# Kernel tuning notes

Measured on AMD Instinct MI355X. Metric: run time of the kernel, lower is better.

Reference implementation:

```python
import jax, jax.numpy as jnp
import numpy as np

B, L, S, D, H = 32, 256, 64, 128, 4
DH = D // H
EPS = 1e-5


def _uniform(k, shape, scale):
    return jax.random.uniform(k, shape, jnp.float32, -scale, scale)


def setup_inputs() -> dict:
    key = jax.random.key(0)
    ks = jax.random.split(key, 12)
    sc = 1.0 / np.sqrt(D)
    return {
        "h_wq": jax.random.normal(ks[0], (B, L, D), jnp.float32),
        "h_all": jax.random.normal(ks[1], (B, L, S, D), jnp.float32),
        "station_id": jax.random.randint(ks[2], (B,), 0, S),
        "adj": jax.random.randint(ks[3], (S, S), 0, 2).astype(jnp.float32),
        "in_proj_w": _uniform(ks[4], (3 * D, D), sc),
        "in_proj_b": _uniform(ks[5], (3 * D,), sc),
        "out_w": _uniform(ks[6], (D, D), sc),
        "out_b": _uniform(ks[7], (D,), sc),
        "gate_w": _uniform(ks[8], (D, 2 * D), 1.0 / np.sqrt(2 * D)),
        "gate_b": _uniform(ks[9], (D,), 1.0 / np.sqrt(2 * D)),
        "ln_g": jnp.ones((D,), jnp.float32),
        "ln_b": jnp.zeros((D,), jnp.float32),
        "alpha": jnp.asarray(0.1, jnp.float32),
    }


def _allowed_mask(adj, station_id):
    # allowed[b, s] == True  <=> station s may attend as key for sample b
    sid = station_id.astype(jnp.int32)
    allowed = adj[sid] > 0.0                                  # [B, S]
    self_oh = jax.nn.one_hot(sid, adj.shape[0], dtype=bool)   # [B, S]
    allowed = allowed & ~self_oh                              # exclude self
    # fallback-to-all for rows with no neighbor (still excluding self)
    no_nb = ~jnp.any(allowed, axis=1, keepdims=True)
    allowed = jnp.where(no_nb, ~self_oh, allowed)
    # final safety: if STILL empty (S==1 edge case), allow self
    no_nb2 = ~jnp.any(allowed, axis=1, keepdims=True)
    allowed = allowed | (no_nb2 & self_oh)
    return allowed


def _forward(h_wq, h_all, station_id, adj, in_proj_w, in_proj_b,
             out_w, out_b, gate_w, gate_b, ln_g, ln_b, alpha):
    b, l, d = h_wq.shape
    s = h_all.shape[2]
    qw, kw, vw = jnp.split(in_proj_w, 3, axis=0)
    qb, kb, vb = jnp.split(in_proj_b, 3, axis=0)

    q = (h_wq @ qw.T + qb).reshape(b, l, H, DH)        # [B,L,H,DH]
    k = (h_all @ kw.T + kb).reshape(b, l, s, H, DH)    # [B,L,S,H,DH]
    v = (h_all @ vw.T + vb).reshape(b, l, s, H, DH)

    scores = jnp.einsum('blhd,blshd->blhs', q, k) / np.sqrt(DH)  # [B,L,H,S]
    allowed = _allowed_mask(adj, station_id)                     # [B,S]
    scores = jnp.where(allowed[:, None, None, :], scores, -jnp.inf)
    w = jax.nn.softmax(scores, axis=-1)

    ctx = jnp.einsum('blhs,blshd->blhd', w, v).reshape(b, l, d)
    ctx = ctx @ out_w.T + out_b                                  # out_proj

    g = jax.nn.sigmoid(jnp.concatenate([h_wq, ctx], axis=-1) @ gate_w.T + gate_b)
    y = h_wq + alpha * (g * ctx)                                 # dropout = eval mode

    mu = jnp.mean(y, axis=-1, keepdims=True)
    var = jnp.mean(jnp.square(y - mu), axis=-1, keepdims=True)
    return (y - mu) * jax.lax.rsqrt(var + EPS) * ln_g + ln_b


def reference(h_wq, h_all, station_id, adj, in_proj_w, in_proj_b,
              out_w, out_b, gate_w, gate_b, ln_g, ln_b, alpha):
    return _forward(h_wq, h_all, station_id, adj, in_proj_w, in_proj_b,
                    out_w, out_b, gate_w, gate_b, ln_g, ln_b, alpha)
```

## Files before the change

kernel.cpp:

```cpp
#include <hip/hip_runtime.h>
#include <math.h>

#define B_   32
#define L_   256
#define S_   64
#define D_   128
#define NTOK (B_*L_)

__global__ __launch_bounds__(256) void fused_kernel(
        const float* __restrict__ h_wq,  const float* __restrict__ h_all,
        const int* __restrict__ station_id, const float* __restrict__ adj,
        const float* __restrict__ in_proj_w, const float* __restrict__ in_proj_b,
        const float* __restrict__ out_w,  const float* __restrict__ out_b,
        const float* __restrict__ gate_w, const float* __restrict__ gate_b,
        const float* __restrict__ ln_g,   const float* __restrict__ ln_b,
        const float* __restrict__ alpha,  float* __restrict__ out) {
    __shared__ float X[4*132];
    __shared__ float QK[4*528];
    __shared__ float A[4*528];
    __shared__ float cb[4][4];
    __shared__ int   lst[64];
    __shared__ int   cnt_s;

    const int t0  = blockIdx.x * 4;
    const int b   = t0 >> 8;
    const int tid = threadIdx.x;
    const int wv  = tid >> 6, lane = tid & 63;
    const int d   = tid & 127, pr = tid >> 7;
    const int tA  = 2*pr, tB = 2*pr + 1;
    const float scale = 0.17677669529663687f;

    if (tid < 64) {
        int sid = station_id[b];
        int s = tid;
        bool av = (adj[sid*S_ + s] > 0.0f) && (s != sid);
        unsigned long long m = __ballot(av);
        if (m == 0ull) { av = (s != sid); m = __ballot(av); }
        if (m == 0ull) { av = (s == sid); m = __ballot(av); }
        int idx = __popcll(m & ((1ull << s) - 1ull));
        if (av) lst[idx] = s;
        if (s == 0) cnt_s = __popcll(m);
    }
    if (tid < 128) {
        int tok = tid >> 5, d4 = tid & 31;
        *(float4*)&X[tok*132 + d4*4] =
            *(const float4*)(h_wq + (size_t)(t0 + tok)*128 + d4*4);
    }
    __syncthreads();

    {
        const float4* wrow = (const float4*)(in_proj_w + (size_t)d*128);
        const float qb = in_proj_b[d];
        float a0 = qb, a1 = qb;
        const float* x0 = &X[tA*132];
        const float* x1 = &X[tB*132];
        #pragma unroll 8
        for (int j4 = 0; j4 < 32; ++j4) {
            float4 w  = wrow[j4];
            float4 u0 = *(const float4*)(x0 + j4*4);
            float4 u1 = *(const float4*)(x1 + j4*4);
            a0 += w.x*u0.x + w.y*u0.y + w.z*u0.z + w.w*u0.w;
            a1 += w.x*u1.x + w.y*u1.y + w.z*u1.z + w.w*u1.w;
        }
        A[tA*132 + d] = a0;
        A[tB*132 + d] = a1;
    }
    __syncthreads();

    {
        const float* q0 = &A[tA*132];
        const float* q1 = &A[tB*132];
        #pragma unroll
        for (int h = 0; h < 4; ++h) {
            float a0 = 0.f, a1 = 0.f;
            const float* wcol = in_proj_w + (size_t)(128 + h*32)*128 + d;
            #pragma unroll 8
            for (int j = 0; j < 32; ++j) {
                float w = wcol[(size_t)j*128];
                a0 += w * q0[h*32 + j];
                a1 += w * q1[h*32 + j];
            }
            QK[tA*528 + h*132 + d] = a0 * scale;
            QK[tB*528 + h*132 + d] = a1 * scale;
        }
    }
    if (tid < 16) {
        int tok = tid >> 2, h = tid & 3;
        float s = 0.f;
        for (int j = 0; j < 32; ++j)
            s += A[tok*132 + h*32 + j] * in_proj_b[128 + h*32 + j];
        cb[tok][h] = s * scale;
    }
    __syncthreads();

    {
        const int g = lane >> 4, lg = lane & 15;
        const float4 qa  = *(const float4*)&QK[wv*528 + g*132 + 8*lg];
        const float4 qb2 = *(const float4*)&QK[wv*528 + g*132 + 8*lg + 4];
        const float cbg = cb[wv][g];
        const int cnt = cnt_s;
        const float* rowbase = h_all + (size_t)(t0 + wv)*(S_*D_) + 8*lg;

        float mg = -INFINITY, ls = 0.f;
        float4 ua = {0,0,0,0}, ub = {0,0,0,0};
        int i = 0;
        for (; i + 2 <= cnt; i += 2) {
            const float* rp0 = rowbase + lst[i]*D_;
            const float* rp1 = rowbase + lst[i+1]*D_;
            float4 xa0 = *(const float4*)rp0, xb0 = *(const float4*)(rp0 + 4);
            float4 xa1 = *(const float4*)rp1, xb1 = *(const float4*)(rp1 + 4);
            float p0 = qa.x*xa0.x + qa.y*xa0.y + qa.z*xa0.z + qa.w*xa0.w
                     + qb2.x*xb0.x + qb2.y*xb0.y + qb2.z*xb0.z + qb2.w*xb0.w;
            float p1 = qa.x*xa1.x + qa.y*xa1.y + qa.z*xa1.z + qa.w*xa1.w
                     + qb2.x*xb1.x + qb2.y*xb1.y + qb2.z*xb1.z + qb2.w*xb1.w;
            p0 += __shfl_xor(p0, 8, 16);  p1 += __shfl_xor(p1, 8, 16);
            p0 += __shfl_xor(p0, 4, 16);  p1 += __shfl_xor(p1, 4, 16);
            p0 += __shfl_xor(p0, 2, 16);  p1 += __shfl_xor(p1, 2, 16);
            p0 += __shfl_xor(p0, 1, 16);  p1 += __shfl_xor(p1, 1, 16);
            float s0 = p0 + cbg, s1 = p1 + cbg;
            float n = fmaxf(mg, fmaxf(s0, s1));
            float r  = __expf(mg - n);
            float w0 = __expf(s0 - n);
            float w1 = __expf(s1 - n);
            ls = ls*r + w0 + w1;
            ua.x = ua.x*r + w0*xa0.x + w1*xa1.x;
            ua.y = ua.y*r + w0*xa0.y + w1*xa1.y;
            ua.z = ua.z*r + w0*xa0.z + w1*xa1.z;
            ua.w = ua.w*r + w0*xa0.w + w1*xa1.w;
            ub.x = ub.x*r + w0*xb0.x + w1*xb1.x;
            ub.y = ub.y*r + w0*xb0.y + w1*xb1.y;
            ub.z = ub.z*r + w0*xb0.z + w1*xb1.z;
            ub.w = ub.w*r + w0*xb0.w + w1*xb1.w;
            mg = n;
        }
        if (i < cnt) {
            const float* rp0 = rowbase + lst[i]*D_;
            float4 xa0 = *(const float4*)rp0, xb0 = *(const float4*)(rp0 + 4);
            float p0 = qa.x*xa0.x + qa.y*xa0.y + qa.z*xa0.z + qa.w*xa0.w
                     + qb2.x*xb0.x + qb2.y*xb0.y + qb2.z*xb0.z + qb2.w*xb0.w;
            p0 += __shfl_xor(p0, 8, 16);
            p0 += __shfl_xor(p0, 4, 16);
            p0 += __shfl_xor(p0, 2, 16);
            p0 += __shfl_xor(p0, 1, 16);
            float s0 = p0 + cbg;
            float n = fmaxf(mg, s0);
            float r = __expf(mg - n), w0 = __expf(s0 - n);
            ls = ls*r + w0;
            ua.x = ua.x*r + w0*xa0.x; ua.y = ua.y*r + w0*xa0.y;
            ua.z = ua.z*r + w0*xa0.z; ua.w = ua.w*r + w0*xa0.w;
            ub.x = ub.x*r + w0*xb0.x; ub.y = ub.y*r + w0*xb0.y;
            ub.z = ub.z*r + w0*xb0.z; ub.w = ub.w*r + w0*xb0.w;
        }
        float inv = 1.f / ls;
        ua.x *= inv; ua.y *= inv; ua.z *= inv; ua.w *= inv;
        ub.x *= inv; ub.y *= inv; ub.z *= inv; ub.w *= inv;
    __syncthreads();
        *(float4*)&A[wv*528 + g*132 + 8*lg]     = ua;
        *(float4*)&A[wv*528 + g*132 + 8*lg + 4] = ub;
    }
    __syncthreads();

    {
        const int h = d >> 5;
        const float4* vwrow = (const float4*)(in_proj_w + (size_t)(256 + d)*128);
        const float vb = in_proj_b[256 + d];
        float a0 = vb, a1 = vb;
        const float* u0 = &A[tA*528 + h*132];
        const float* u1 = &A[tB*528 + h*132];
        #pragma unroll 8
        for (int j4 = 0; j4 < 32; ++j4) {
            float4 w  = vwrow[j4];
            float4 v0 = *(const float4*)(u0 + j4*4);
            float4 v1 = *(const float4*)(u1 + j4*4);
            a0 += w.x*v0.x + w.y*v0.y + w.z*v0.z + w.w*v0.w;
            a1 += w.x*v1.x + w.y*v1.y + w.z*v1.z + w.w*v1.w;
        }
        __syncthreads();
        QK[tA*132 + d] = a0;
        QK[tB*132 + d] = a1;
    }
    __syncthreads();

    {
        const float4* wrow = (const float4*)(out_w + (size_t)d*128);
        const float ob = out_b[d];
        float a0 = ob, a1 = ob;
        const float* c0 = &QK[tA*132];
        const float* c1 = &QK[tB*132];
        #pragma unroll 8
        for (int j4 = 0; j4 < 32; ++j4) {
            float4 w  = wrow[j4];
            float4 v0 = *(const float4*)(c0 + j4*4);
            float4 v1 = *(const float4*)(c1 + j4*4);
            a0 += w.x*v0.x + w.y*v0.y + w.z*v0.z + w.w*v0.w;
            a1 += w.x*v1.x + w.y*v1.y + w.z*v1.z + w.w*v1.w;
        }
        __syncthreads();
        A[tA*132 + d] = a0;
        A[tB*132 + d] = a1;
    }
    __syncthreads();

    {
        const float4* wrow = (const float4*)(gate_w + (size_t)d*256);
        const float gb = gate_b[d];
        float g0 = gb, g1 = gb;
        const float* x0 = &X[tA*132];
        const float* x1 = &X[tB*132];
        const float* o0 = &A[tA*132];
        const float* o1 = &A[tB*132];
        #pragma unroll 4
        for (int j4 = 0; j4 < 32; ++j4) {
            float4 wx = wrow[j4];
            float4 wo = wrow[32 + j4];
            float4 vx0 = *(const float4*)(x0 + j4*4);
            float4 vx1 = *(const float4*)(x1 + j4*4);
            float4 vo0 = *(const float4*)(o0 + j4*4);
            float4 vo1 = *(const float4*)(o1 + j4*4);
            g0 += wx.x*vx0.x + wx.y*vx0.y + wx.z*vx0.z + wx.w*vx0.w
                + wo.x*vo0.x + wo.y*vo0.y + wo.z*vo0.z + wo.w*vo0.w;
            g1 += wx.x*vx1.x + wx.y*vx1.y + wx.z*vx1.z + wx.w*vx1.w
                + wo.x*vo1.x + wo.y*vo1.y + wo.z*vo1.z + wo.w*vo1.w;
        }
        const float al = alpha[0];
        float s0 = 1.0f / (1.0f + __expf(-g0));
        float s1 = 1.0f / (1.0f + __expf(-g1));
        QK[528 + tA*132 + d] = x0[d] + al * s0 * o0[d];
        QK[528 + tB*132 + d] = x1[d] + al * s1 * o1[d];
    }
    __syncthreads();

    {
        float y0 = QK[528 + wv*132 + lane];
        float y1 = QK[528 + wv*132 + 64 + lane];
        float s = y0 + y1;
        #pragma unroll
        for (int o = 32; o >= 1; o >>= 1) s += __shfl_xor(s, o);
        float mu = s * (1.0f/128.0f);
        float d0 = y0 - mu, d1 = y1 - mu;
        float v = d0*d0 + d1*d1;
        #pragma unroll
        for (int o = 32; o >= 1; o >>= 1) v += __shfl_xor(v, o);
        float rs = rsqrtf(v*(1.0f/128.0f) + 1e-5f);
        out[(size_t)(t0 + wv)*128 + lane]      = d0*rs*ln_g[lane]    + ln_b[lane];
        out[(size_t)(t0 + wv)*128 + 64 + lane] = d1*rs*ln_g[64+lane] + ln_b[64+lane];
    }
}

extern "C" void kernel_launch(void* const* d_in, const int* in_sizes, int n_in,
                              void* d_out, int out_size, void* d_ws, size_t ws_size,
                              hipStream_t stream) {
    const float* h_wq       = (const float*)d_in[0];
    const float* h_all      = (const float*)d_in[1];
    const int*   station_id = (const int*)  d_in[2];
    const float* adj        = (const float*)d_in[3];
    const float* in_proj_w  = (const float*)d_in[4];
    const float* in_proj_b  = (const float*)d_in[5];
    const float* out_w      = (const float*)d_in[6];
    const float* out_b      = (const float*)d_in[7];
    const float* gate_w     = (const float*)d_in[8];
    const float* gate_b     = (const float*)d_in[9];
    const float* ln_g       = (const float*)d_in[10];
    const float* ln_b       = (const float*)d_in[11];
    const float* alpha      = (const float*)d_in[12];
    float* out = (float*)d_out;

    fused_kernel<<<NTOK/4, 256, 0, stream>>>(
        h_wq, h_all, station_id, adj, in_proj_w, in_proj_b,
        out_w, out_b, gate_w, gate_b, ln_g, ln_b, alpha, out);
}
```

Baseline: 495.1 us.

## Compute attention scores lane-per-key with wave-wide softmax instead of online softmax

Replaces the serial online-softmax loop, where 16-lane groups walked the allowed keys two at a time, with a two-pass scheme. In the first pass each lane computes the full 128-wide score of one key for all four heads, and wave-wide shuffle reductions produce the softmax max and sum. The normalized weights are written to shared memory, and a second loop over keys accumulates the weighted value rows with lanes spanning the feature dimension. This removes the long dependent exp/rescale chain, but it reads each h_all row twice and the first pass uses strided per-lane row loads. A now-unneeded __syncthreads in the V projection stage is also dropped.

After: 516.0 us. +4.2%, slower.

```diff
diff --git a/kernel.cpp b/kernel.cpp
--- a/kernel.cpp
+++ b/kernel.cpp
@@ -94,69 +94,66 @@
     __syncthreads();
 
     {
-        const int g = lane >> 4, lg = lane & 15;
-        const float4 qa  = *(const float4*)&QK[wv*528 + g*132 + 8*lg];
-        const float4 qb2 = *(const float4*)&QK[wv*528 + g*132 + 8*lg + 4];
-        const float cbg = cb[wv][g];
         const int cnt = cnt_s;
-        const float* rowbase = h_all + (size_t)(t0 + wv)*(S_*D_) + 8*lg;
-
-        float mg = -INFINITY, ls = 0.f;
-        float4 ua = {0,0,0,0}, ub = {0,0,0,0};
-        int i = 0;
-        for (; i + 2 <= cnt; i += 2) {
-            const float* rp0 = rowbase + lst[i]*D_;
-            const float* rp1 = rowbase + lst[i+1]*D_;
-            float4 xa0 = *(const float4*)rp0, xb0 = *(const float4*)(rp0 + 4);
-            float4 xa1 = *(const float4*)rp1, xb1 = *(const float4*)(rp1 + 4);
-            float p0 = qa.x*xa0.x + qa.y*xa0.y + qa.z*xa0.z + qa.w*xa0.w
-                     + qb2.x*xb0.x + qb2.y*xb0.y + qb2.z*xb0.z + qb2.w*xb0.w;
-            float p1 = qa.x*xa1.x + qa.y*xa1.y + qa.z*xa1.z + qa.w*xa1.w
-                     + qb2.x*xb1.x + qb2.y*xb1.y + qb2.z*xb1.z + qb2.w*xb1.w;
-            p0 += __shfl_xor(p0, 8, 16);  p1 += __shfl_xor(p1, 8, 16);
-            p0 += __shfl_xor(p0, 4, 16);  p1 += __shfl_xor(p1, 4, 16);
-            p0 += __shfl_xor(p0, 2, 16);  p1 += __shfl_xor(p1, 2, 16);
-            p0 += __shfl_xor(p0, 1, 16);  p1 += __shfl_xor(p1, 1, 16);
-            float s0 = p0 + cbg, s1 = p1 + cbg;
-            float n = fmaxf(mg, fmaxf(s0, s1));
-            float r  = __expf(mg - n);
-            float w0 = __expf(s0 - n);
-            float w1 = __expf(s1 - n);
-            ls = ls*r + w0 + w1;
-            ua.x = ua.x*r + w0*xa0.x + w1*xa1.x;
-            ua.y = ua.y*r + w0*xa0.y + w1*xa1.y;
-            ua.z = ua.z*r + w0*xa0.z + w1*xa1.z;
-            ua.w = ua.w*r + w0*xa0.w + w1*xa1.w;
-            ub.x = ub.x*r + w0*xb0.x + w1*xb1.x;
-            ub.y = ub.y*r + w0*xb0.y + w1*xb1.y;
-            ub.z = ub.z*r + w0*xb0.z + w1*xb1.z;
-            ub.w = ub.w*r + w0*xb0.w + w1*xb1.w;
-            mg = n;
-        }
-        if (i < cnt) {
-            const float* rp0 = rowbase + lst[i]*D_;
-            float4 xa0 = *(const float4*)rp0, xb0 = *(const float4*)(rp0 + 4);
-            float p0 = qa.x*xa0.x + qa.y*xa0.y + qa.z*xa0.z + qa.w*xa0.w
-                     + qb2.x*xb0.x + qb2.y*xb0.y + qb2.z*xb0.z + qb2.w*xb0.w;
-            p0 += __shfl_xor(p0, 8, 16);
-            p0 += __shfl_xor(p0, 4, 16);
-            p0 += __shfl_xor(p0, 2, 16);
-            p0 += __shfl_xor(p0, 1, 16);
-            float s0 = p0 + cbg;
-            float n = fmaxf(mg, s0);
-            float r = __expf(mg - n), w0 = __expf(s0 - n);
-            ls = ls*r + w0;
-            ua.x = ua.x*r + w0*xa0.x; ua.y = ua.y*r + w0*xa0.y;
-            ua.z = ua.z*r + w0*xa0.z; ua.w = ua.w*r + w0*xa0.w;
-            ub.x = ub.x*r + w0*xb0.x; ub.y = ub.y*r + w0*xb0.y;
-            ub.z = ub.z*r + w0*xb0.z; ub.w = ub.w*r + w0*xb0.w;
-        }
-        float inv = 1.f / ls;
-        ua.x *= inv; ua.y *= inv; ua.z *= inv; ua.w *= inv;
-        ub.x *= inv; ub.y *= inv; ub.z *= inv; ub.w *= inv;
-    __syncthreads();
-        *(float4*)&A[wv*528 + g*132 + 8*lg]     = ua;
-        *(float4*)&A[wv*528 + g*132 + 8*lg + 4] = ub;
+        const int ridx = lst[lane < cnt ? lane : 0];
+        const float* rp  = h_all + (size_t)(t0 + wv)*(S_*D_) + (size_t)ridx*D_;
+        const float* qkb = &QK[wv*528];
+
+        float s0 = cb[wv][0], s1 = cb[wv][1], s2 = cb[wv][2], s3 = cb[wv][3];
+        #pragma unroll 8
+        for (int j4 = 0; j4 < 32; ++j4) {
+            float4 x  = *(const float4*)(rp + j4*4);
+            float4 w0 = *(const float4*)(qkb + 0*132 + j4*4);
+            float4 w1 = *(const float4*)(qkb + 1*132 + j4*4);
+            float4 w2 = *(const float4*)(qkb + 2*132 + j4*4);
+            float4 w3 = *(const float4*)(qkb + 3*132 + j4*4);
+            s0 += w0.x*x.x + w0.y*x.y + w0.z*x.z + w0.w*x.w;
+            s1 += w1.x*x.x + w1.y*x.y + w1.z*x.z + w1.w*x.w;
+            s2 += w2.x*x.x + w2.y*x.y + w2.z*x.z + w2.w*x.w;
+            s3 += w3.x*x.x + w3.y*x.y + w3.z*x.z + w3.w*x.w;
+        }
+        const bool act = (lane < cnt);
+        if (!act) { s0 = s1 = s2 = s3 = -INFINITY; }
+
+        float m0 = s0, m1 = s1, m2 = s2, m3 = s3;
+        #pragma unroll
+        for (int o = 32; o >= 1; o >>= 1) {
+            m0 = fmaxf(m0, __shfl_xor(m0, o));
+            m1 = fmaxf(m1, __shfl_xor(m1, o));
+            m2 = fmaxf(m2, __shfl_xor(m2, o));
+            m3 = fmaxf(m3, __shfl_xor(m3, o));
+        }
+        float p0 = act ? __expf(s0 - m0) : 0.f;
+        float p1 = act ? __expf(s1 - m1) : 0.f;
+        float p2 = act ? __expf(s2 - m2) : 0.f;
+        float p3 = act ? __expf(s3 - m3) : 0.f;
+        float q0 = p0, q1 = p1, q2 = p2, q3 = p3;
+        #pragma unroll
+        for (int o = 32; o >= 1; o >>= 1) {
+            q0 += __shfl_xor(q0, o);
+            q1 += __shfl_xor(q1, o);
+            q2 += __shfl_xor(q2, o);
+            q3 += __shfl_xor(q3, o);
+        }
+        float4 wv4;
+        wv4.x = p0 / q0; wv4.y = p1 / q1; wv4.z = p2 / q2; wv4.w = p3 / q3;
+        *(float4*)&QK[wv*528 + lane*4] = wv4;
+
+        float u00=0,u01=0,u10=0,u11=0,u20=0,u21=0,u30=0,u31=0;
+        const float* base = h_all + (size_t)(t0 + wv)*(S_*D_);
+        for (int i = 0; i < cnt; ++i) {
+            const float* rb = base + (size_t)lst[i]*D_;
+            float x0 = rb[lane], x1 = rb[64 + lane];
+            float4 w = *(const float4*)&QK[wv*528 + i*4];
+            u00 += w.x*x0; u01 += w.x*x1;
+            u10 += w.y*x0; u11 += w.y*x1;
+            u20 += w.z*x0; u21 += w.z*x1;
+            u30 += w.w*x0; u31 += w.w*x1;
+        }
+        A[wv*528 + 0*132 + lane] = u00;  A[wv*528 + 0*132 + 64 + lane] = u01;
+        A[wv*528 + 1*132 + lane] = u10;  A[wv*528 + 1*132 + 64 + lane] = u11;
+        A[wv*528 + 2*132 + lane] = u20;  A[wv*528 + 2*132 + 64 + lane] = u21;
+        A[wv*528 + 3*132 + lane] = u30;  A[wv*528 + 3*132 + 64 + lane] = u31;
     }
     __syncthreads();
 
@@ -175,7 +172,6 @@
             a0 += w.x*v0.x + w.y*v0.y + w.z*v0.z + w.w*v0.w;
             a1 += w.x*v1.x + w.y*v1.y + w.z*v1.z + w.w*v1.w;
         }
-        __syncthreads();
         QK[tA*132 + d] = a0;
         QK[tB*132 + d] = a1;
     }
```
